# Kernel optimization log

Measured on AMD Instinct MI355X. Metric: run time of the kernel, lower is better.

Reference implementation:

```python
import jax, jax.numpy as jnp
import numpy as np

D_MODEL = 1024
N_HEADS = 16
D_HEAD = D_MODEL // N_HEADS


def setup_inputs() -> dict:
    key = jax.random.key(0)
    ks = jax.random.split(key, 5)
    s_in = 1.0 / np.sqrt(D_MODEL)
    x = jax.random.normal(ks[0], (4, 2048, D_MODEL), dtype=jnp.float32)
    W_qkv = jax.random.uniform(ks[1], (D_MODEL, 3 * D_MODEL), jnp.float32, -s_in, s_in)
    b_qkv = jax.random.uniform(ks[2], (3 * D_MODEL,), jnp.float32, -s_in, s_in)
    W_out = jax.random.uniform(ks[3], (D_MODEL, D_MODEL), jnp.float32, -s_in, s_in)
    b_out = jax.random.uniform(ks[4], (D_MODEL,), jnp.float32, -s_in, s_in)
    return {"x": x, "W_qkv": W_qkv, "b_qkv": b_qkv, "W_out": W_out, "b_out": b_out}


def reference(x, W_qkv, b_qkv, W_out, b_out):
    B, T, C = x.shape
    qkv = x @ W_qkv + b_qkv                       # [B,T,3C]
    q, k, v = jnp.split(qkv, 3, axis=-1)
    # [B,T,C] -> [B,H,T,Dh]
    def heads(t):
        return t.reshape(B, T, N_HEADS, D_HEAD).transpose(0, 2, 1, 3)
    q, k, v = heads(q), heads(k), heads(v)
    scale = 1.0 / np.sqrt(D_HEAD).astype(np.float32)
    attn = jnp.einsum('bhqd,bhkd->bhqk', q, k) * scale   # [B,H,T,T]
    causal = jnp.tril(jnp.ones((T, T), dtype=bool))
    attn = jnp.where(causal, attn, -jnp.inf)
    attn_weights = jax.nn.softmax(attn, axis=-1)
    out = jnp.einsum('bhqk,bhkd->bhqd', attn_weights, v)  # [B,H,T,Dh]
    out = out.transpose(0, 2, 1, 3).reshape(B, T, C)
    return out @ W_out + b_out
```

## Files before the change

kernel.cpp:

```cpp
#include <hip/hip_runtime.h>
#include <hip/hip_bf16.h>

#define BATCH   4
#define SEQ     2048
#define DMODEL  1024
#define NHEADS  16
#define DHEAD   64
#define MROWS   (BATCH*SEQ)
#define QKV_N   (3*DMODEL)
#define NEG_BIG (-1.0e30f)
#define WS_NEED ((size_t)MROWS * 2*DMODEL * sizeof(__hip_bfloat16))
#define SCALE_Q 0.18033688011112042f

using bf16 = __hip_bfloat16;
typedef __attribute__((ext_vector_type(8))) short short8;
typedef __attribute__((ext_vector_type(4))) float floatx4;

__device__ __align__(16) unsigned short g_wqT[QKV_N * DMODEL];
__device__ __align__(16) unsigned short g_woT[DMODEL * DMODEL];
__device__ __align__(16) unsigned short g_xb [MROWS * DMODEL];

__device__ __forceinline__ unsigned short f2bf_rne(float f) {
    union { bf16 b; unsigned short u; } t;
    t.b = __float2bfloat16(f);
    return t.u;
}

__device__ __forceinline__ void gload_lds16(const void* g, void* l) {
    __builtin_amdgcn_global_load_lds(
        (const __attribute__((address_space(1))) unsigned*)g,
        (__attribute__((address_space(3))) unsigned*)l, 16, 0, 0);
}

__global__ __launch_bounds__(256) void cast_x(const float* __restrict__ x) {
    const size_t i = ((size_t)blockIdx.x*256 + threadIdx.x)*8;
    const float4 a = *(const float4*)(x + i);
    const float4 b = *(const float4*)(x + i + 4);
    union { uint4 u4; unsigned short us[8]; } o;
    o.us[0]=f2bf_rne(a.x); o.us[1]=f2bf_rne(a.y); o.us[2]=f2bf_rne(a.z); o.us[3]=f2bf_rne(a.w);
    o.us[4]=f2bf_rne(b.x); o.us[5]=f2bf_rne(b.y); o.us[6]=f2bf_rne(b.z); o.us[7]=f2bf_rne(b.w);
    *(uint4*)(g_xb + i) = o.u4;
}

__global__ __launch_bounds__(256) void transcast_w2(
    const float* __restrict__ Wq, const float* __restrict__ Wo)
{
    const int bx = blockIdx.x;
    const float* W;
    unsigned short* dst;
    int N, n0;
    if (bx < 48) { W = Wq; dst = g_wqT; N = QKV_N;  n0 = bx * 64; }
    else         { W = Wo; dst = g_woT; N = DMODEL; n0 = (bx - 48) * 64; }
    const int k0 = blockIdx.y * 64;

    __shared__ unsigned short T[64][72];
    const int tid = threadIdx.x;
    const int r = tid >> 2, c0 = (tid & 3) * 16;

#pragma unroll
    for (int it = 0; it < 4; ++it) {
        const float4 v = *(const float4*)(W + (size_t)(k0 + r)*N + n0 + c0 + it*4);
        T[r][c0 + it*4 + 0] = f2bf_rne(v.x);
        T[r][c0 + it*4 + 1] = f2bf_rne(v.y);
        T[r][c0 + it*4 + 2] = f2bf_rne(v.z);
        T[r][c0 + it*4 + 3] = f2bf_rne(v.w);
    }
    __syncthreads();
    const int nr = tid >> 2, kc0 = (tid & 3) * 16;
#pragma unroll
    for (int it = 0; it < 2; ++it) {
        union { uint4 u4; unsigned short us[8]; } o;
#pragma unroll
        for (int j = 0; j < 8; j++) o.us[j] = T[kc0 + it*8 + j][nr];
        *(uint4*)(dst + (size_t)(n0 + nr)*DMODEL + k0 + kc0 + it*8) = o.u4;
    }
}

__global__ __launch_bounds__(512, 2) void qkv_proj(
    const float* __restrict__ bias, bf16* __restrict__ Qo,
    bf16* __restrict__ Ko, bf16* __restrict__ VT)
{
    const unsigned short* A  = g_xb;
    const unsigned short* BT = g_wqT;
    constexpr int NBN = 12;
    constexpr int NWG = 32 * NBN;

    __shared__ __align__(16) char smem[131072];
    char* const sA = smem;
    char* const sB = smem + 65536;

    const int orig = blockIdx.x;
    const int wgid = (orig & 7) * (NWG >> 3) + (orig >> 3);
    const int bm = wgid / NBN, bn = wgid % NBN;

    const int tid  = threadIdx.x;
    const int w    = tid >> 6, lane = tid & 63;
    const int m16  = lane & 15, quad = lane >> 4;
    const int rw   = w >> 2, cw = w & 3;

    const int rL = lane >> 2;
    const int cD = (lane & 3) ^ ((lane >> 3) & 3);
    const unsigned short* gA = A  + (size_t)(bm*256 + rL)*DMODEL + cD*8;
    const unsigned short* gB = BT + (size_t)(bn*256 + rL)*DMODEL + cD*8;

    const int laneRd = m16*64 + (quad ^ ((m16 >> 1) & 3))*16;

    floatx4 acc[8][4];
#pragma unroll
    for (int i = 0; i < 8; ++i)
#pragma unroll
        for (int j = 0; j < 4; ++j) {
            acc[i][j][0]=0.f; acc[i][j][1]=0.f; acc[i][j][2]=0.f; acc[i][j][3]=0.f;
        }

    auto stA = [&](int buf, int rg, int kh, int k0) {
        gload_lds16(gA + (size_t)(rg*16)*DMODEL + k0 + kh*32,
                    sA + buf*32768 + (rg*2 + kh)*1024);
    };
    auto stB = [&](int buf, int rg, int kh, int k0) {
        gload_lds16(gB + (size_t)(rg*16)*DMODEL + k0 + kh*32,
                    sB + buf*32768 + (rg*2 + kh)*1024);
    };

    stB(0, 2*w, 0, 0);   stB(0, 2*w+1, 0, 0);
    stA(0, w,   0, 0);   stA(0, w,   1, 0);
    stA(0, 8+w, 0, 0);   stA(0, 8+w, 1, 0);
    stB(0, 2*w, 1, 0);   stB(0, 2*w+1, 1, 0);
    asm volatile("s_waitcnt vmcnt(0)" ::: "memory");
    __builtin_amdgcn_s_barrier();

    const int NT = DMODEL / 64;
    for (int t = 0; t < NT; ++t) {
        const int  buf = t & 1;
        const int  k1  = (t + 1) * 64;
        const bool st  = (t + 1 < NT);
        char* const Ab = sA + buf*32768;
        char* const Bb = sB + buf*32768;

        short8 bf[4], af[4];

#pragma unroll
        for (int j = 0; j < 4; ++j)
            bf[j] = *(const short8*)(Bb + ((cw*4 + j)*2 + 0)*1024 + laneRd);
#pragma unroll
        for (int i = 0; i < 4; ++i)
            af[i] = *(const short8*)(Ab + ((rw*8 + i)*2 + 0)*1024 + laneRd);
        if (st) { stB(buf^1, 2*w, 0, k1); stB(buf^1, 2*w+1, 0, k1); }
        __builtin_amdgcn_s_barrier();
        __builtin_amdgcn_s_setprio(1);
#pragma unroll
        for (int i = 0; i < 4; ++i)
#pragma unroll
            for (int j = 0; j < 4; ++j)
                acc[i][j] = __builtin_amdgcn_mfma_f32_16x16x32_bf16(af[i], bf[j], acc[i][j], 0, 0, 0);
        __builtin_amdgcn_s_setprio(0);
        if (st) { asm volatile("s_waitcnt vmcnt(4)" ::: "memory"); }
        else    { asm volatile("s_waitcnt vmcnt(2)" ::: "memory"); }
        __builtin_amdgcn_s_barrier();

#pragma unroll
        for (int i = 0; i < 4; ++i)
            af[i] = *(const short8*)(Ab + ((rw*8 + 4 + i)*2 + 0)*1024 + laneRd);
        if (st) { stA(buf^1, w, 0, k1); stA(buf^1, w, 1, k1); }
        __builtin_amdgcn_s_barrier();
        __builtin_amdgcn_s_setprio(1);
#pragma unroll
        for (int i = 0; i < 4; ++i)
#pragma unroll
            for (int j = 0; j < 4; ++j)
                acc[4+i][j] = __builtin_amdgcn_mfma_f32_16x16x32_bf16(af[i], bf[j], acc[4+i][j], 0, 0, 0);
        __builtin_amdgcn_s_setprio(0);
        if (st) { asm volatile("s_waitcnt vmcnt(4)" ::: "memory"); }
        else    { asm volatile("s_waitcnt vmcnt(0)" ::: "memory"); }
        __builtin_amdgcn_s_barrier();

#pragma unroll
        for (int j = 0; j < 4; ++j)
            bf[j] = *(const short8*)(Bb + ((cw*4 + j)*2 + 1)*1024 + laneRd);
#pragma unroll
        for (int i = 0; i < 4; ++i)
            af[i] = *(const short8*)(Ab + ((rw*8 + i)*2 + 1)*1024 + laneRd);
        if (st) { stA(buf^1, 8+w, 0, k1); stA(buf^1, 8+w, 1, k1); }
        __builtin_amdgcn_s_barrier();
        __builtin_amdgcn_s_setprio(1);
#pragma unroll
        for (int i = 0; i < 4; ++i)
#pragma unroll
            for (int j = 0; j < 4; ++j)
                acc[i][j] = __builtin_amdgcn_mfma_f32_16x16x32_bf16(af[i], bf[j], acc[i][j], 0, 0, 0);
        __builtin_amdgcn_s_setprio(0);
        if (st) { asm volatile("s_waitcnt vmcnt(6)" ::: "memory"); }
        else    { asm volatile("s_waitcnt vmcnt(0)" ::: "memory"); }
        __builtin_amdgcn_s_barrier();

#pragma unroll
        for (int i = 0; i < 4; ++i)
            af[i] = *(const short8*)(Ab + ((rw*8 + 4 + i)*2 + 1)*1024 + laneRd);
        if (st) { stB(buf^1, 2*w, 1, k1); stB(buf^1, 2*w+1, 1, k1); }
        __builtin_amdgcn_s_barrier();
        __builtin_amdgcn_s_setprio(1);
#pragma unroll
        for (int i = 0; i < 4; ++i)
#pragma unroll
            for (int j = 0; j < 4; ++j)
                acc[4+i][j] = __builtin_amdgcn_mfma_f32_16x16x32_bf16(af[i], bf[j], acc[4+i][j], 0, 0, 0);
        __builtin_amdgcn_s_setprio(0);
        if (st) {
            asm volatile("s_waitcnt vmcnt(4)" ::: "memory");
            __builtin_amdgcn_s_barrier();
        }
    }

    float bv[4];
#pragma unroll
    for (int j = 0; j < 4; ++j)
        bv[j] = bias[bn*256 + cw*64 + j*16 + m16];

    const int seg = bn >> 2;
    if (seg < 2) {
        bf16* Cout = seg ? Ko : Qo;
        const float sc = seg ? 1.0f : SCALE_Q;
#pragma unroll
        for (int mf = 0; mf < 8; ++mf)
#pragma unroll
            for (int r = 0; r < 4; ++r) {
                const int gm = bm*256 + rw*128 + mf*16 + quad*4 + r;
#pragma unroll
                for (int j = 0; j < 4; ++j) {
                    const int cc = (bn*256 + cw*64 + j*16 + m16) & 1023;
                    Cout[(size_t)gm*DMODEL + cc] =
                        __float2bfloat16((acc[mf][j][r] + bv[j]) * sc);
                }
            }
    } else {
#pragma unroll
        for (int mf = 0; mf < 8; ++mf) {
            const int gm0 = bm*256 + rw*128 + mf*16 + quad*4;
            const int bb = gm0 >> 11, t0 = gm0 & 2047;
#pragma unroll
            for (int j = 0; j < 4; ++j) {
                const int cv = ((bn & 3)*256 + cw*64 + j*16 + m16);
                const int hh = cv >> 6, dd = cv & 63;
                union { unsigned long long u8; unsigned short us[4]; } o;
#pragma unroll
                for (int r = 0; r < 4; ++r)
                    o.us[r] = f2bf_rne(acc[mf][j][r] + bv[j]);
                *(unsigned long long*)(VT
                    + ((size_t)((bb*NHEADS + hh)*DHEAD + dd))*SEQ + t0) = o.u8;
            }
        }
    }
}

__global__ __launch_bounds__(512, 2) void out_proj(
    const void* __restrict__ Av, const float* __restrict__ bias, float* C)
{
    const unsigned short* A  = (const unsigned short*)Av;
    const unsigned short* BT = g_woT;
    constexpr int NBN = 8;
    constexpr int NWG = NBN * 32;

    __shared__ __align__(16) char smem[98304];
    char* const sA = smem;
    char* const sB = smem + 65536;

    const int orig = blockIdx.x;
    const int wgid = (orig & 7) * (NWG >> 3) + (orig >> 3);
    const int bm = wgid / NBN, bn = wgid % NBN;

    const int tid  = threadIdx.x;
    const int w    = tid >> 6, lane = tid & 63;
    const int m16  = lane & 15, quad = lane >> 4;
    const int rw   = w >> 1, cw = w & 1;

    const int rL = lane >> 2;
    const int cD = (lane & 3) ^ ((lane >> 3) & 3);
    const unsigned short* gA = A  + (size_t)(bm*256 + rL)*DMODEL + cD*8;
    const unsigned short* gB = BT + (size_t)(bn*128 + rL)*DMODEL + cD*8;

    const int laneRd = m16*64 + (quad ^ ((m16 >> 1) & 3))*16;

    floatx4 acc[2][2][4];
#pragma unroll
    for (int q = 0; q < 2; ++q)
#pragma unroll
        for (int i = 0; i < 2; ++i)
#pragma unroll
            for (int j = 0; j < 4; ++j) {
                acc[q][i][j][0]=0.f; acc[q][i][j][1]=0.f;
                acc[q][i][j][2]=0.f; acc[q][i][j][3]=0.f;
            }

    auto stageA = [&](int buf, int a, int k0) {
        const int rg = 4*a + (w >> 1), kh = w & 1;
        gload_lds16(gA + (size_t)(rg*16)*DMODEL + k0 + kh*32,
                    sA + buf*32768 + (rg*2 + kh)*1024);
    };
    auto stageB = [&](int buf, int b, int k0) {
        const int rg = 4*b + (w >> 1), kh = w & 1;
        gload_lds16(gB + (size_t)(rg*16)*DMODEL + k0 + kh*32,
                    sB + buf*16384 + (rg*2 + kh)*1024);
    };

    stageB(0, 0, 0); stageB(0, 1, 0);
    stageA(0, 0, 0); stageA(0, 1, 0); stageA(0, 2, 0); stageA(0, 3, 0);
    asm volatile("s_waitcnt vmcnt(0)" ::: "memory");
    __builtin_amdgcn_s_barrier();

    const int NT = DMODEL / 64;
    for (int t = 0; t < NT; ++t) {
        const int  buf = t & 1;
        const int  k1  = (t + 1) * 64;
        const bool st  = (t + 1 < NT);
        char* const Ab = sA + buf*32768;
        char* const Bb = sB + buf*16384;

        short8 bf[4][2], af[2][2];
#pragma unroll
        for (int j = 0; j < 4; ++j)
#pragma unroll
            for (int kh = 0; kh < 2; ++kh)
                bf[j][kh] = *(const short8*)(Bb + ((cw*4 + j)*2 + kh)*1024 + laneRd);
#pragma unroll
        for (int i = 0; i < 2; ++i)
#pragma unroll
            for (int kh = 0; kh < 2; ++kh)
                af[i][kh] = *(const short8*)(Ab + ((rw*2 + i)*2 + kh)*1024 + laneRd);

        if (st) { stageB(buf^1, 0, k1); stageB(buf^1, 1, k1);
                  stageA(buf^1, 0, k1); stageA(buf^1, 1, k1); }
        __builtin_amdgcn_s_barrier();

        __builtin_amdgcn_s_setprio(1);
#pragma unroll
        for (int i = 0; i < 2; ++i)
#pragma unroll
            for (int j = 0; j < 4; ++j) {
                acc[0][i][j] = __builtin_amdgcn_mfma_f32_16x16x32_bf16(
                    af[i][0], bf[j][0], acc[0][i][j], 0, 0, 0);
                acc[0][i][j] = __builtin_amdgcn_mfma_f32_16x16x32_bf16(
                    af[i][1], bf[j][1], acc[0][i][j], 0, 0, 0);
            }
        __builtin_amdgcn_s_setprio(0);

        if (st) { asm volatile("s_waitcnt vmcnt(4)" ::: "memory"); }
        else    { asm volatile("s_waitcnt vmcnt(0)" ::: "memory"); }
        __builtin_amdgcn_s_barrier();

#pragma unroll
        for (int i = 0; i < 2; ++i)
#pragma unroll
            for (int kh = 0; kh < 2; ++kh)
                af[i][kh] = *(const short8*)(Ab + ((8 + rw*2 + i)*2 + kh)*1024 + laneRd);

        if (st) { stageA(buf^1, 2, k1); stageA(buf^1, 3, k1); }
        __builtin_amdgcn_s_barrier();

        __builtin_amdgcn_s_setprio(1);
#pragma unroll
        for (int i = 0; i < 2; ++i)
#pragma unroll
            for (int j = 0; j < 4; ++j) {
                acc[1][i][j] = __builtin_amdgcn_mfma_f32_16x16x32_bf16(
                    af[i][0], bf[j][0], acc[1][i][j], 0, 0, 0);
                acc[1][i][j] = __builtin_amdgcn_mfma_f32_16x16x32_bf16(
                    af[i][1], bf[j][1], acc[1][i][j], 0, 0, 0);
            }
        __builtin_amdgcn_s_setprio(0);

        if (st) { asm volatile("s_waitcnt vmcnt(2)" ::: "memory"); }
        else    { asm volatile("s_waitcnt vmcnt(0)" ::: "memory"); }
        __builtin_amdgcn_s_barrier();
    }

    float bv[4];
#pragma unroll
    for (int j = 0; j < 4; ++j)
        bv[j] = bias[bn*128 + cw*64 + j*16 + m16];

#pragma unroll
    for (int q = 0; q < 2; ++q)
#pragma unroll
        for (int i = 0; i < 2; ++i)
#pragma unroll
            for (int r = 0; r < 4; ++r) {
                const int gm = bm*256 + q*128 + rw*32 + i*16 + quad*4 + r;
#pragma unroll
                for (int j = 0; j < 4; ++j) {
                    const int cc = bn*128 + cw*64 + j*16 + m16;
                    C[(size_t)gm*DMODEL + cc] = acc[q][i][j][r] + bv[j];
                }
            }
}

__global__ __launch_bounds__(256, 3) void attn_mfma6(
    const bf16* __restrict__ Qg, const bf16* __restrict__ Kg,
    const bf16* __restrict__ VTg, bf16* __restrict__ Og)
{
    __shared__ alignas(16) unsigned short Kt[2][64][72];
    __shared__ alignas(16) unsigned short Vt[64][72];
    __shared__ alignas(16) unsigned short Ps[4][32][72];

    const int L  = blockIdx.x;
    const int qt = 15 - (L >> 6);
    const int bh = L & 63;
    const int b  = bh >> 4, h = bh & 15;

    const int tid = threadIdx.x;
    const int w = tid >> 6, lane = tid & 63;
    const int m16 = lane & 15, quad = lane >> 4;
    const int sr = tid >> 2, sc0 = (tid & 3) * 8;
    const size_t bhs = (size_t)(b*NHEADS + h);

    const int nkt = 2*qt + 2;
    const int qrow0 = qt*128 + w*32;

    short8 qf[2][2];
#pragma unroll
    for (int i = 0; i < 2; ++i)
#pragma unroll
        for (int c = 0; c < 2; ++c)
            qf[i][c] = *(const short8*)(Qg + (size_t)(b*SEQ + qrow0 + i*16 + m16)*DMODEL
                                        + h*DHEAD + c*32 + quad*8);

    floatx4 of[2][4];
    float mrow[2], lrow[2];
#pragma unroll
    for (int i = 0; i < 2; ++i) {
        mrow[i] = NEG_BIG; lrow[i] = 0.f;
#pragma unroll
        for (int nt = 0; nt < 4; ++nt) { of[i][nt][0]=0.f; of[i][nt][1]=0.f; of[i][nt][2]=0.f; of[i][nt][3]=0.f; }
    }

    {
        const bf16* kp = Kg  + (size_t)(b*SEQ + sr)*DMODEL + h*DHEAD + sc0;
        const bf16* vp = VTg + (bhs*DHEAD + sr)*SEQ + sc0;
        const uint4 a0 = *(const uint4*)kp, a1 = *(const uint4*)(kp + 32);
        const uint4 b0 = *(const uint4*)vp, b1 = *(const uint4*)(vp + 32);
        *(uint4*)&Kt[0][sr][sc0]      = a0;
        *(uint4*)&Kt[0][sr][sc0 + 32] = a1;
        *(uint4*)&Vt[sr][sc0]         = b0;
        *(uint4*)&Vt[sr][sc0 + 32]    = b1;
        __syncthreads();
    }

    for (int kt = 0; kt < nkt; ++kt) {
        const int buf = kt & 1;
        const int k064 = kt * 64;
        const bool pre = (kt + 1 < nkt);
        uint4 kr0, kr1, vr0, vr1;
        if (pre) {
            const bf16* kp = Kg  + (size_t)(b*SEQ + k064 + 64 + sr)*DMODEL + h*DHEAD + sc0;
            const bf16* vp = VTg + (bhs*DHEAD + sr)*SEQ + k064 + 64 + sc0;
            kr0 = *(const uint4*)kp; kr1 = *(const uint4*)(kp + 32);
            vr0 = *(const uint4*)vp; vr1 = *(const uint4*)(vp + 32);
        }

        floatx4 sf[2][4];
#pragma unroll
        for (int t4 = 0; t4 < 4; ++t4) {
            const short8 kf0 = *(const short8*)&Kt[buf][t4*16 + m16][quad*8];
            const short8 kf1 = *(const short8*)&Kt[buf][t4*16 + m16][32 + quad*8];
#pragma unroll
            for (int i = 0; i < 2; ++i) {
                floatx4 a; a[0]=0.f; a[1]=0.f; a[2]=0.f; a[3]=0.f;
                a = __builtin_amdgcn_mfma_f32_16x16x32_bf16(kf0, qf[i][0], a, 0, 0, 0);
                a = __builtin_amdgcn_mfma_f32_16x16x32_bf16(kf1, qf[i][1], a, 0, 0, 0);
                sf[i][t4] = a;
            }
        }

        const bool need_mask = (k064 + 63 > qrow0);
#pragma unroll
        for (int i = 0; i < 2; ++i) {
            if (need_mask) {
                const int qg = qrow0 + i*16 + m16;
#pragma unroll
                for (int t4 = 0; t4 < 4; ++t4)
#pragma unroll
                    for (int r = 0; r < 4; ++r)
                        if (k064 + t4*16 + quad*4 + r > qg) sf[i][t4][r] = NEG_BIG;
            }
            float mx = sf[i][0][0];
#pragma unroll
            for (int t4 = 0; t4 < 4; ++t4)
#pragma unroll
                for (int r = 0; r < 4; ++r) mx = fmaxf(mx, sf[i][t4][r]);
            mx = fmaxf(mx, __shfl_xor(mx, 16));
            mx = fmaxf(mx, __shfl_xor(mx, 32));

            if (__any(mx > mrow[i] + 8.f)) {
                const float mnew  = fmaxf(mrow[i], mx);
                const float alpha = exp2f(mrow[i] - mnew);
                mrow[i] = mnew;
                lrow[i] *= alpha;
#pragma unroll
                for (int nt = 0; nt < 4; ++nt)
#pragma unroll
                    for (int r = 0; r < 4; ++r) of[i][nt][r] *= alpha;
            }

            float rs = 0.f;
#pragma unroll
            for (int t4 = 0; t4 < 4; ++t4) {
#pragma unroll
                for (int r = 0; r < 4; ++r) {
                    const float pv = exp2f(sf[i][t4][r] - mrow[i]);
                    sf[i][t4][r] = pv;
                    rs += pv;
                }
            }
            rs += __shfl_xor(rs, 16);
            rs += __shfl_xor(rs, 32);
            lrow[i] += rs;

#pragma unroll
            for (int t4 = 0; t4 < 4; ++t4) {
                union { unsigned long long u8; unsigned short us[4]; } o;
#pragma unroll
                for (int r = 0; r < 4; ++r) o.us[r] = f2bf_rne(sf[i][t4][r]);
                *(unsigned long long*)&Ps[w][i*16 + m16][t4*16 + quad*4] = o.u8;
            }
        }

        short8 pf[2][2];
#pragma unroll
        for (int i = 0; i < 2; ++i)
#pragma unroll
            for (int c = 0; c < 2; ++c)
                pf[i][c] = *(const short8*)&Ps[w][i*16 + m16][c*32 + quad*8];
#pragma unroll
        for (int nt = 0; nt < 4; ++nt) {
            const short8 vf0 = *(const short8*)&Vt[nt*16 + m16][quad*8];
            const short8 vf1 = *(const short8*)&Vt[nt*16 + m16][32 + quad*8];
#pragma unroll
            for (int i = 0; i < 2; ++i) {
                of[i][nt] = __builtin_amdgcn_mfma_f32_16x16x32_bf16(vf0, pf[i][0], of[i][nt], 0, 0, 0);
                of[i][nt] = __builtin_amdgcn_mfma_f32_16x16x32_bf16(vf1, pf[i][1], of[i][nt], 0, 0, 0);
            }
        }

        __syncthreads();
        if (pre) {
            *(uint4*)&Kt[buf^1][sr][sc0]      = kr0;
            *(uint4*)&Kt[buf^1][sr][sc0 + 32] = kr1;
            *(uint4*)&Vt[sr][sc0]             = vr0;
            *(uint4*)&Vt[sr][sc0 + 32]        = vr1;
        }
        __syncthreads();
    }

#pragma unroll
    for (int i = 0; i < 2; ++i) {
        const float rl = 1.f / fmaxf(lrow[i], 1e-20f);
        const size_t rowbase = (size_t)(b*SEQ + qrow0 + i*16 + m16)*DMODEL + h*DHEAD;
#pragma unroll
        for (int nt = 0; nt < 4; ++nt) {
            union { unsigned long long u8; unsigned short us[4]; } o;
#pragma unroll
            for (int r = 0; r < 4; ++r) o.us[r] = f2bf_rne(of[i][nt][r] * rl);
            *(unsigned long long*)(Og + rowbase + nt*16 + quad*4) = o.u8;
        }
    }
}

__global__ void diag_fill(float* out, int n, float val) {
    int i = blockIdx.x*blockDim.x + threadIdx.x;
    if (i < n) out[i] = val;
}

extern "C" void kernel_launch(void* const* d_in, const int* in_sizes, int n_in,
                              void* d_out, int out_size, void* d_ws, size_t ws_size,
                              hipStream_t stream) {
    const float* x     = (const float*)d_in[0];
    const float* W_qkv = (const float*)d_in[1];
    const float* b_qkv = (const float*)d_in[2];
    const float* W_out = (const float*)d_in[3];
    const float* b_out = (const float*)d_in[4];

    if (ws_size < WS_NEED) {
        const float val = 100.f + (float)(ws_size >> 20);
        diag_fill<<<(out_size + 255)/256, 256, 0, stream>>>((float*)d_out, out_size, val);
        return;
    }

    bf16* Qb  = (bf16*)d_out;
    bf16* VTb = (bf16*)d_out + (size_t)MROWS*DMODEL;
    bf16* Kb  = (bf16*)d_ws;
    bf16* Ob  = (bf16*)d_ws + (size_t)MROWS*DMODEL;

    cast_x<<<MROWS*DMODEL/2048, 256, 0, stream>>>(x);
    {
        dim3 g(64, DMODEL/64);
        transcast_w2<<<g, 256, 0, stream>>>(W_qkv, W_out);
    }
    qkv_proj<<<384, 512, 0, stream>>>(b_qkv, Qb, Kb, VTb);
    attn_mfma6<<<1024, 256, 0, stream>>>(Qb, Kb, VTb, Ob);
    out_proj<<<256, 512, 0, stream>>>(Ob, b_out, (float*)d_out);
}
```

Measured before the change: 264.8 us.

## Fold softmax row sum into PV MFMA via ones row; reorder GEMM prefetch

The attention kernel appends a 16-row tile to the V shared buffer whose first row is all ones (bf16 1.0), so an extra MFMA column accumulates the softmax denominator. This removes the per-row exp sum and cross-lane shuffles, and the final normalizer is read by a shuffle from that accumulator. It costs extra MFMAs, registers and shared memory, and the sum is now taken over bf16-rounded probabilities. Separately, the QKV GEMM changes the order of its async global-to-LDS prefetches and drops two intermediate vmcnt waits, which risks a race unless the barriers and remaining waits still cover the loads.

```diff
diff --git a/kernel.cpp b/kernel.cpp
--- a/kernel.cpp
+++ b/kernel.cpp
@@ -122,10 +122,10 @@
                     sB + buf*32768 + (rg*2 + kh)*1024);
     };
 
-    stB(0, 2*w, 0, 0);   stB(0, 2*w+1, 0, 0);
-    stA(0, w,   0, 0);   stA(0, w,   1, 0);
-    stA(0, 8+w, 0, 0);   stA(0, 8+w, 1, 0);
-    stB(0, 2*w, 1, 0);   stB(0, 2*w+1, 1, 0);
+    stA(0, w, 0, 0);   stA(0, 8+w, 0, 0);
+    stB(0, 2*w, 0, 0); stB(0, 2*w+1, 0, 0);
+    stA(0, w, 1, 0);   stA(0, 8+w, 1, 0);
+    stB(0, 2*w, 1, 0); stB(0, 2*w+1, 1, 0);
     asm volatile("s_waitcnt vmcnt(0)" ::: "memory");
     __builtin_amdgcn_s_barrier();
 
@@ -145,7 +145,7 @@
 #pragma unroll
         for (int i = 0; i < 4; ++i)
             af[i] = *(const short8*)(Ab + ((rw*8 + i)*2 + 0)*1024 + laneRd);
-        if (st) { stB(buf^1, 2*w, 0, k1); stB(buf^1, 2*w+1, 0, k1); }
+        if (st) { stA(buf^1, w, 0, k1); stA(buf^1, 8+w, 0, k1); }
         __builtin_amdgcn_s_barrier();
         __builtin_amdgcn_s_setprio(1);
 #pragma unroll
@@ -154,14 +154,12 @@
             for (int j = 0; j < 4; ++j)
                 acc[i][j] = __builtin_amdgcn_mfma_f32_16x16x32_bf16(af[i], bf[j], acc[i][j], 0, 0, 0);
         __builtin_amdgcn_s_setprio(0);
-        if (st) { asm volatile("s_waitcnt vmcnt(4)" ::: "memory"); }
-        else    { asm volatile("s_waitcnt vmcnt(2)" ::: "memory"); }
         __builtin_amdgcn_s_barrier();
 
 #pragma unroll
         for (int i = 0; i < 4; ++i)
             af[i] = *(const short8*)(Ab + ((rw*8 + 4 + i)*2 + 0)*1024 + laneRd);
-        if (st) { stA(buf^1, w, 0, k1); stA(buf^1, w, 1, k1); }
+        if (st) { stB(buf^1, 2*w, 0, k1); stB(buf^1, 2*w+1, 0, k1); }
         __builtin_amdgcn_s_barrier();
         __builtin_amdgcn_s_setprio(1);
 #pragma unroll
@@ -180,7 +178,7 @@
 #pragma unroll
         for (int i = 0; i < 4; ++i)
             af[i] = *(const short8*)(Ab + ((rw*8 + i)*2 + 1)*1024 + laneRd);
-        if (st) { stA(buf^1, 8+w, 0, k1); stA(buf^1, 8+w, 1, k1); }
+        if (st) { stA(buf^1, w, 1, k1); stA(buf^1, 8+w, 1, k1); }
         __builtin_amdgcn_s_barrier();
         __builtin_amdgcn_s_setprio(1);
 #pragma unroll
@@ -189,8 +187,6 @@
             for (int j = 0; j < 4; ++j)
                 acc[i][j] = __builtin_amdgcn_mfma_f32_16x16x32_bf16(af[i], bf[j], acc[i][j], 0, 0, 0);
         __builtin_amdgcn_s_setprio(0);
-        if (st) { asm volatile("s_waitcnt vmcnt(6)" ::: "memory"); }
-        else    { asm volatile("s_waitcnt vmcnt(0)" ::: "memory"); }
         __builtin_amdgcn_s_barrier();
 
 #pragma unroll
@@ -393,12 +389,12 @@
             }
 }
 
-__global__ __launch_bounds__(256, 3) void attn_mfma6(
+__global__ __launch_bounds__(256, 3) void attn_mfma7(
     const bf16* __restrict__ Qg, const bf16* __restrict__ Kg,
     const bf16* __restrict__ VTg, bf16* __restrict__ Og)
 {
     __shared__ alignas(16) unsigned short Kt[2][64][72];
-    __shared__ alignas(16) unsigned short Vt[64][72];
+    __shared__ alignas(16) unsigned short Vt[80][72];
     __shared__ alignas(16) unsigned short Ps[4][32][72];
 
     const int L  = blockIdx.x;
@@ -423,13 +419,18 @@
             qf[i][c] = *(const short8*)(Qg + (size_t)(b*SEQ + qrow0 + i*16 + m16)*DMODEL
                                         + h*DHEAD + c*32 + quad*8);
 
-    floatx4 of[2][4];
-    float mrow[2], lrow[2];
+    floatx4 of[2][5];
+    float mrow[2];
 #pragma unroll
     for (int i = 0; i < 2; ++i) {
-        mrow[i] = NEG_BIG; lrow[i] = 0.f;
-#pragma unroll
-        for (int nt = 0; nt < 4; ++nt) { of[i][nt][0]=0.f; of[i][nt][1]=0.f; of[i][nt][2]=0.f; of[i][nt][3]=0.f; }
+        mrow[i] = NEG_BIG;
+#pragma unroll
+        for (int nt = 0; nt < 5; ++nt) { of[i][nt][0]=0.f; of[i][nt][1]=0.f; of[i][nt][2]=0.f; of[i][nt][3]=0.f; }
+    }
+
+    for (int idx = tid; idx < 16*72; idx += 256) {
+        const int r = idx / 72, c = idx % 72;
+        Vt[64 + r][c] = (r == 0) ? (unsigned short)0x3F80 : (unsigned short)0;
     }
 
     {
@@ -493,26 +494,17 @@
                 const float mnew  = fmaxf(mrow[i], mx);
                 const float alpha = exp2f(mrow[i] - mnew);
                 mrow[i] = mnew;
-                lrow[i] *= alpha;
-#pragma unroll
-                for (int nt = 0; nt < 4; ++nt)
+#pragma unroll
+                for (int nt = 0; nt < 5; ++nt)
 #pragma unroll
                     for (int r = 0; r < 4; ++r) of[i][nt][r] *= alpha;
             }
 
-            float rs = 0.f;
-#pragma unroll
-            for (int t4 = 0; t4 < 4; ++t4) {
-#pragma unroll
-                for (int r = 0; r < 4; ++r) {
-                    const float pv = exp2f(sf[i][t4][r] - mrow[i]);
-                    sf[i][t4][r] = pv;
-                    rs += pv;
-                }
-            }
-            rs += __shfl_xor(rs, 16);
-            rs += __shfl_xor(rs, 32);
-            lrow[i] += rs;
+#pragma unroll
+            for (int t4 = 0; t4 < 4; ++t4)
+#pragma unroll
+                for (int r = 0; r < 4; ++r)
+                    sf[i][t4][r] = exp2f(sf[i][t4][r] - mrow[i]);
 
 #pragma unroll
             for (int t4 = 0; t4 < 4; ++t4) {
@@ -530,7 +522,7 @@
             for (int c = 0; c < 2; ++c)
                 pf[i][c] = *(const short8*)&Ps[w][i*16 + m16][c*32 + quad*8];
 #pragma unroll
-        for (int nt = 0; nt < 4; ++nt) {
+        for (int nt = 0; nt < 5; ++nt) {
             const short8 vf0 = *(const short8*)&Vt[nt*16 + m16][quad*8];
             const short8 vf1 = *(const short8*)&Vt[nt*16 + m16][32 + quad*8];
 #pragma unroll
@@ -552,7 +544,8 @@
 
 #pragma unroll
     for (int i = 0; i < 2; ++i) {
-        const float rl = 1.f / fmaxf(lrow[i], 1e-20f);
+        const float lsum = __shfl(of[i][4][0], m16);
+        const float rl = 1.f / fmaxf(lsum, 1e-20f);
         const size_t rowbase = (size_t)(b*SEQ + qrow0 + i*16 + m16)*DMODEL + h*DHEAD;
 #pragma unroll
         for (int nt = 0; nt < 4; ++nt) {
@@ -595,6 +588,6 @@
         transcast_w2<<<g, 256, 0, stream>>>(W_qkv, W_out);
     }
     qkv_proj<<<384, 512, 0, stream>>>(b_qkv, Qb, Kb, VTb);
-    attn_mfma6<<<1024, 256, 0, stream>>>(Qb, Kb, VTb, Ob);
+    attn_mfma7<<<1024, 256, 0, stream>>>(Qb, Kb, VTb, Ob);
     out_proj<<<256, 512, 0, stream>>>(Ob, b_out, (float*)d_out);
 }
```

Result: no change. 266.9 us (+0.8%).
